# Optimization experiments

Hardware: AMD Instinct MI355X
Metric: run time of the kernel (lower is better)

Reference implementation:

```python
import jax, jax.numpy as jnp
import numpy as np

N_NODES = 100000


def gcn_conv(x, W, b, src, dst, deg_inv_sqrt):
    # x: [N, Cin], W: [Cin, Cout]. PyG GCNConv: transform then normalized aggregate.
    h = x @ W  # [N, Cout]
    norm = deg_inv_sqrt[src] * deg_inv_sqrt[dst]  # [E']
    msg = h[src] * norm[:, None]  # gather + scale
    out = jax.ops.segment_sum(msg, dst, num_segments=N_NODES)
    return out + b


def setup_inputs() -> dict:
    key = jax.random.key(0)
    ks = jax.random.split(key, 8)
    C = 256
    E = 3200000
    x = jax.random.normal(ks[0], (N_NODES, C), dtype=jnp.float32)
    edge_index = jax.random.randint(ks[1], (2, E), 0, N_NODES, dtype=jnp.int64)
    s = 1.0 / np.sqrt(C)
    W1 = jax.random.uniform(ks[2], (C, C), jnp.float32, -s, s)
    b1 = jnp.zeros((C,), jnp.float32)
    W2 = jax.random.uniform(ks[3], (C, C), jnp.float32, -s, s)
    b2 = jnp.zeros((C,), jnp.float32)
    Wl = jax.random.uniform(ks[4], (C, 1), jnp.float32, -s, s)
    bl = jnp.zeros((1,), jnp.float32)
    return {"x": x, "edge_index": edge_index, "W1": W1, "b1": b1,
            "W2": W2, "b2": b2, "Wl": Wl, "bl": bl}


def reference(x, edge_index, W1, b1, W2, b2, Wl, bl):
    # add self-loops once (shared by both conv layers)
    loops = jnp.arange(N_NODES, dtype=edge_index.dtype)
    src = jnp.concatenate([edge_index[0], loops])
    dst = jnp.concatenate([edge_index[1], loops])
    # symmetric normalization: deg counts incoming edges incl. self-loops
    deg = jax.ops.segment_sum(jnp.ones_like(dst, dtype=x.dtype), dst,
                              num_segments=N_NODES)
    deg_inv_sqrt = jax.lax.rsqrt(deg)  # deg >= 1 due to self-loops
    h = jax.nn.relu(gcn_conv(x, W1, b1, src, dst, deg_inv_sqrt))
    h = jax.nn.relu(gcn_conv(h, W2, b2, src, dst, deg_inv_sqrt))
    return h @ Wl + bl  # [N, 1]
```

## Files before the change

### kernel.cpp

```cpp
#include <hip/hip_runtime.h>

#define NN 100000
#define CC 256
#define EE 3200000

typedef __attribute__((ext_vector_type(8))) short bf16x8;
typedef __attribute__((ext_vector_type(4))) float f32x4;
typedef __attribute__((ext_vector_type(4))) _Float16 f16x4;

__device__ __forceinline__ float4 f4add(float4 a, float4 b) {
  return make_float4(a.x + b.x, a.y + b.y, a.z + b.z, a.w + b.w);
}

__device__ __forceinline__ unsigned short f2bf(float f) {
  unsigned u = __float_as_uint(f);
  unsigned r = (u + 0x7fffu + ((u >> 16) & 1u)) >> 16;
  return (unsigned short)r;
}
__device__ __forceinline__ float bf2f(unsigned short h) {
  return __uint_as_float(((unsigned)h) << 16);
}

__global__ void k_deg(const int* __restrict__ dst, int* __restrict__ cnt, int n) {
  int i = blockIdx.x * blockDim.x + threadIdx.x;
  int stride = gridDim.x * blockDim.x;
  for (; i < n; i += stride) {
    unsigned d = (unsigned)dst[i];
    if (d < NN) atomicAdd(&cnt[d], 1);
  }
}

__global__ void k_dis(const int* __restrict__ cnt, float* __restrict__ dis, int n) {
  int i = blockIdx.x * blockDim.x + threadIdx.x;
  if (i < n) dis[i] = 1.0f / sqrtf((float)(cnt[i] + 1));
}

__global__ void k_scan_local(const int* __restrict__ cnt, int* __restrict__ offs,
                             int* __restrict__ bsum, int n) {
  __shared__ int wsum[16];
  int t = threadIdx.x;
  int idx = blockIdx.x * 1024 + t;
  int lane = t & 63, wv = t >> 6;
  int v = (idx < n) ? cnt[idx] : 0;
  int x = v;
#pragma unroll
  for (int d = 1; d < 64; d <<= 1) {
    int y = __shfl_up(x, d, 64);
    if (lane >= d) x += y;
  }
  if (lane == 63) wsum[wv] = x;
  __syncthreads();
  int wpre = 0, total = 0;
#pragma unroll
  for (int w = 0; w < 16; ++w) {
    int s = wsum[w];
    if (w < wv) wpre += s;
    total += s;
  }
  if (idx < n) offs[idx] = wpre + x - v;
  if (t == 0) bsum[blockIdx.x] = total;
}

__global__ void k_scan_bsum(const int* __restrict__ bsum, int* __restrict__ bbase, int nb) {
  __shared__ int wsum[2];
  int t = threadIdx.x;
  int lane = t & 63, wv = t >> 6;
  int v = (t < nb) ? bsum[t] : 0;
  int x = v;
#pragma unroll
  for (int d = 1; d < 64; d <<= 1) {
    int y = __shfl_up(x, d, 64);
    if (lane >= d) x += y;
  }
  if (lane == 63) wsum[wv] = x;
  __syncthreads();
  int pre = (wv == 1) ? wsum[0] : 0;
  if (t < nb) bbase[t] = pre + x - v;
  if (t == nb - 1) bbase[nb] = pre + x;
}

__global__ void k_scan_add(int* __restrict__ offs, const int* __restrict__ bbase,
                           int n, int nb) {
  int i = blockIdx.x * 256 + threadIdx.x;
  if (i < n) offs[i] += bbase[i >> 10];
  if (i == 0) offs[n] = bbase[nb];
}

__global__ void k_scatter(const int* __restrict__ src, const int* __restrict__ dst,
                          const int* __restrict__ offs, int* __restrict__ fill,
                          int* __restrict__ csr, int n) {
  int i = blockIdx.x * blockDim.x + threadIdx.x;
  int stride = gridDim.x * blockDim.x;
  for (; i < n; i += stride) {
    unsigned d = (unsigned)dst[i];
    unsigned s = (unsigned)src[i];
    if (d < NN && s < NN) {
      int p = offs[d] + atomicAdd(&fill[d], 1);
      csr[p] = (int)s;
    }
  }
}

__global__ void k_wsplit(const float* __restrict__ W, unsigned short* __restrict__ WTh,
                         unsigned short* __restrict__ WTl) {
  int k = blockIdx.x, n = threadIdx.x;
  float w = W[k * CC + n];
  unsigned short h = f2bf(w);
  unsigned short l = f2bf(w - bf2f(h));
  WTh[n * CC + k] = h;
  WTl[n * CC + k] = l;
}

#define LDA 40

__global__ __launch_bounds__(512) void k_gemm_mfma(
    const float* __restrict__ A, const unsigned short* __restrict__ WTh,
    const unsigned short* __restrict__ WTl, const float* __restrict__ dis,
    _Float16* __restrict__ Out, int M) {
  __shared__ unsigned short Ah[128 * LDA], Al[128 * LDA];
  __shared__ unsigned short Bh[256 * LDA], Bl[256 * LDA];
  const int tid = threadIdx.x;
  const int wave = tid >> 6, lane = tid & 63;
  const int quad = lane >> 4, l16 = lane & 15;
  const int wm = wave >> 2, wn = wave & 3;
  const int row0 = blockIdx.x * 128;

  f32x4 acc[4][4];
#pragma unroll
  for (int i = 0; i < 4; ++i)
#pragma unroll
    for (int j = 0; j < 4; ++j) acc[i][j] = (f32x4){0.f, 0.f, 0.f, 0.f};

  for (int k0 = 0; k0 < CC; k0 += 32) {
#pragma unroll
    for (int q = 0; q < 2; ++q) {
      int idx = tid + 512 * q;
      int r = idx >> 3;
      int c4 = (idx & 7) << 2;
      int gr = row0 + r;
      float4 v = make_float4(0.f, 0.f, 0.f, 0.f);
      if (gr < M) v = *(const float4*)&A[(size_t)gr * CC + k0 + c4];
      ushort4 hv, lv;
      hv.x = f2bf(v.x); lv.x = f2bf(v.x - bf2f(hv.x));
      hv.y = f2bf(v.y); lv.y = f2bf(v.y - bf2f(hv.y));
      hv.z = f2bf(v.z); lv.z = f2bf(v.z - bf2f(hv.z));
      hv.w = f2bf(v.w); lv.w = f2bf(v.w - bf2f(hv.w));
      *(ushort4*)&Ah[r * LDA + c4] = hv;
      *(ushort4*)&Al[r * LDA + c4] = lv;
    }
#pragma unroll
    for (int q = 0; q < 4; ++q) {
      int idx = tid + 512 * q;
      int r = idx >> 3;
      int c4 = (idx & 7) << 2;
      const size_t g = (size_t)r * CC + k0 + c4;
      *(ushort4*)&Bh[r * LDA + c4] = *(const ushort4*)&WTh[g];
      *(ushort4*)&Bl[r * LDA + c4] = *(const ushort4*)&WTl[g];
    }
    __syncthreads();

    bf16x8 bh[4], bl[4];
#pragma unroll
    for (int j = 0; j < 4; ++j) {
      int br = (wn * 64 + j * 16 + l16) * LDA + quad * 8;
      bh[j] = *(const bf16x8*)&Bh[br];
      bl[j] = *(const bf16x8*)&Bl[br];
    }
#pragma unroll
    for (int i = 0; i < 4; ++i) {
      int ar = (wm * 64 + i * 16 + l16) * LDA + quad * 8;
      bf16x8 ah = *(const bf16x8*)&Ah[ar];
      bf16x8 al = *(const bf16x8*)&Al[ar];
#pragma unroll
      for (int j = 0; j < 4; ++j) {
        acc[i][j] = __builtin_amdgcn_mfma_f32_16x16x32_bf16(ah, bh[j], acc[i][j], 0, 0, 0);
        acc[i][j] = __builtin_amdgcn_mfma_f32_16x16x32_bf16(al, bh[j], acc[i][j], 0, 0, 0);
        acc[i][j] = __builtin_amdgcn_mfma_f32_16x16x32_bf16(ah, bl[j], acc[i][j], 0, 0, 0);
      }
    }
    __syncthreads();
  }

#pragma unroll
  for (int i = 0; i < 4; ++i) {
#pragma unroll
    for (int r4 = 0; r4 < 4; ++r4) {
      int r = row0 + wm * 64 + i * 16 + quad * 4 + r4;
      if (r < M) {
        float sc = dis[r];
#pragma unroll
        for (int j = 0; j < 4; ++j) {
          Out[(size_t)r * CC + wn * 64 + j * 16 + l16] =
              (_Float16)(acc[i][j][r4] * sc);
        }
      }
    }
  }
}

__global__ __launch_bounds__(256) void k_aggregate(
    const _Float16* __restrict__ hs, const int* __restrict__ offs,
    const int* __restrict__ csr, const float* __restrict__ dis,
    const float* __restrict__ bias, float* __restrict__ out, int n) {
  int node = blockIdx.x * 4 + (threadIdx.x >> 6);
  if (node >= n) return;
  int lane = threadIdx.x & 63;
  int c4 = lane << 2;
  int beg = offs[node], end = offs[node + 1];
  f16x4 sv = *(const f16x4*)&hs[(size_t)node * CC + c4];
  float4 a0 = make_float4((float)sv.x, (float)sv.y, (float)sv.z, (float)sv.w);
  float4 a1 = make_float4(0.f, 0.f, 0.f, 0.f);
  float4 a2 = make_float4(0.f, 0.f, 0.f, 0.f);
  float4 a3 = make_float4(0.f, 0.f, 0.f, 0.f);
  int e = beg;
  for (; e + 4 <= end; e += 4) {
    int s0 = csr[e], s1 = csr[e + 1], s2 = csr[e + 2], s3 = csr[e + 3];
    f16x4 v0 = *(const f16x4*)&hs[(size_t)s0 * CC + c4];
    f16x4 v1 = *(const f16x4*)&hs[(size_t)s1 * CC + c4];
    f16x4 v2 = *(const f16x4*)&hs[(size_t)s2 * CC + c4];
    f16x4 v3 = *(const f16x4*)&hs[(size_t)s3 * CC + c4];
    a0.x += (float)v0.x; a0.y += (float)v0.y; a0.z += (float)v0.z; a0.w += (float)v0.w;
    a1.x += (float)v1.x; a1.y += (float)v1.y; a1.z += (float)v1.z; a1.w += (float)v1.w;
    a2.x += (float)v2.x; a2.y += (float)v2.y; a2.z += (float)v2.z; a2.w += (float)v2.w;
    a3.x += (float)v3.x; a3.y += (float)v3.y; a3.z += (float)v3.z; a3.w += (float)v3.w;
  }
  for (; e < end; ++e) {
    int s0 = csr[e];
    f16x4 v0 = *(const f16x4*)&hs[(size_t)s0 * CC + c4];
    a0.x += (float)v0.x; a0.y += (float)v0.y; a0.z += (float)v0.z; a0.w += (float)v0.w;
  }
  float4 acc = f4add(f4add(a0, a1), f4add(a2, a3));
  float sc = dis[node];
  float4 bv = *(const float4*)&bias[c4];
  float4 r;
  r.x = fmaxf(acc.x * sc + bv.x, 0.f);
  r.y = fmaxf(acc.y * sc + bv.y, 0.f);
  r.z = fmaxf(acc.z * sc + bv.z, 0.f);
  r.w = fmaxf(acc.w * sc + bv.w, 0.f);
  *(float4*)&out[(size_t)node * CC + c4] = r;
}

__global__ __launch_bounds__(256) void k_aggregate_final(
    const _Float16* __restrict__ hs, const int* __restrict__ offs,
    const int* __restrict__ csr, const float* __restrict__ dis,
    const float* __restrict__ bias, const float* __restrict__ Wl,
    const float* __restrict__ bl, float* __restrict__ out, int n) {
  int node = blockIdx.x * 4 + (threadIdx.x >> 6);
  if (node >= n) return;
  int lane = threadIdx.x & 63;
  int c4 = lane << 2;
  int beg = offs[node], end = offs[node + 1];
  f16x4 sv = *(const f16x4*)&hs[(size_t)node * CC + c4];
  float4 a0 = make_float4((float)sv.x, (float)sv.y, (float)sv.z, (float)sv.w);
  float4 a1 = make_float4(0.f, 0.f, 0.f, 0.f);
  float4 a2 = make_float4(0.f, 0.f, 0.f, 0.f);
  float4 a3 = make_float4(0.f, 0.f, 0.f, 0.f);
  int e = beg;
  for (; e + 4 <= end; e += 4) {
    int s0 = csr[e], s1 = csr[e + 1], s2 = csr[e + 2], s3 = csr[e + 3];
    f16x4 v0 = *(const f16x4*)&hs[(size_t)s0 * CC + c4];
    f16x4 v1 = *(const f16x4*)&hs[(size_t)s1 * CC + c4];
    f16x4 v2 = *(const f16x4*)&hs[(size_t)s2 * CC + c4];
    f16x4 v3 = *(const f16x4*)&hs[(size_t)s3 * CC + c4];
    a0.x += (float)v0.x; a0.y += (float)v0.y; a0.z += (float)v0.z; a0.w += (float)v0.w;
    a1.x += (float)v1.x; a1.y += (float)v1.y; a1.z += (float)v1.z; a1.w += (float)v1.w;
    a2.x += (float)v2.x; a2.y += (float)v2.y; a2.z += (float)v2.z; a2.w += (float)v2.w;
    a3.x += (float)v3.x; a3.y += (float)v3.y; a3.z += (float)v3.z; a3.w += (float)v3.w;
  }
  for (; e < end; ++e) {
    int s0 = csr[e];
    f16x4 v0 = *(const f16x4*)&hs[(size_t)s0 * CC + c4];
    a0.x += (float)v0.x; a0.y += (float)v0.y; a0.z += (float)v0.z; a0.w += (float)v0.w;
  }
  float4 acc = f4add(f4add(a0, a1), f4add(a2, a3));
  float sc = dis[node];
  float4 bv = *(const float4*)&bias[c4];
  float4 w = *(const float4*)&Wl[c4];
  float s = fmaxf(acc.x * sc + bv.x, 0.f) * w.x +
            fmaxf(acc.y * sc + bv.y, 0.f) * w.y +
            fmaxf(acc.z * sc + bv.z, 0.f) * w.z +
            fmaxf(acc.w * sc + bv.w, 0.f) * w.w;
#pragma unroll
  for (int d = 32; d > 0; d >>= 1) s += __shfl_down(s, d, 64);
  if (lane == 0) out[node] = s + bl[0];
}

extern "C" void kernel_launch(void* const* d_in, const int* in_sizes, int n_in,
                              void* d_out, int out_size, void* d_ws, size_t ws_size,
                              hipStream_t stream) {
  const float* x = (const float*)d_in[0];
  const int* ei = (const int*)d_in[1];
  const float* W1 = (const float*)d_in[2];
  const float* b1 = (const float*)d_in[3];
  const float* W2 = (const float*)d_in[4];
  const float* b2 = (const float*)d_in[5];
  const float* Wl = (const float*)d_in[6];
  const float* bl = (const float*)d_in[7];
  float* out = (float*)d_out;

  const int* src = ei;
  const int* dst = ei + EE;

  char* ws = (char*)d_ws;
  size_t off = 0;
  auto alloc = [&](size_t bytes) {
    char* p = ws + off;
    off = (off + bytes + 255) & ~(size_t)255;
    return p;
  };
  float* dis = (float*)alloc((size_t)NN * 4);
  int* cnt = (int*)alloc((size_t)NN * 4);
  int* offs = (int*)alloc((size_t)(NN + 1) * 4);
  int* scanb = (int*)alloc(1024 * 4);
  int* scanb2 = (int*)alloc(1024 * 4);
  int* csr = (int*)alloc((size_t)EE * 4);
  unsigned short* W1h = (unsigned short*)alloc((size_t)CC * CC * 2);
  unsigned short* W1l = (unsigned short*)alloc((size_t)CC * CC * 2);
  unsigned short* W2h = (unsigned short*)alloc((size_t)CC * CC * 2);
  unsigned short* W2l = (unsigned short*)alloc((size_t)CC * CC * 2);
  _Float16* hsbuf = (_Float16*)alloc((size_t)NN * CC * 2);
  float* h1 = (float*)alloc((size_t)NN * CC * 4);

  hipMemsetAsync(cnt, 0, (size_t)NN * 4, stream);

  k_deg<<<2048, 256, 0, stream>>>(dst, cnt, EE);
  k_dis<<<(NN + 255) / 256, 256, 0, stream>>>(cnt, dis, NN);
  const int nb = (NN + 1023) / 1024;
  k_scan_local<<<nb, 1024, 0, stream>>>(cnt, offs, scanb, NN);
  k_scan_bsum<<<1, 128, 0, stream>>>(scanb, scanb2, nb);
  k_scan_add<<<(NN + 255) / 256, 256, 0, stream>>>(offs, scanb2, NN, nb);
  hipMemsetAsync(cnt, 0, (size_t)NN * 4, stream);
  k_scatter<<<2048, 256, 0, stream>>>(src, dst, offs, cnt, csr, EE);

  k_wsplit<<<CC, CC, 0, stream>>>(W1, W1h, W1l);
  k_wsplit<<<CC, CC, 0, stream>>>(W2, W2h, W2l);

  const int gblocks = (NN + 127) / 128;
  k_gemm_mfma<<<gblocks, 512, 0, stream>>>(x, W1h, W1l, dis, hsbuf, NN);
  k_aggregate<<<(NN + 3) / 4, 256, 0, stream>>>(hsbuf, offs, csr, dis, b1, h1, NN);
  k_gemm_mfma<<<gblocks, 512, 0, stream>>>(h1, W2h, W2l, dis, hsbuf, NN);
  k_aggregate_final<<<(NN + 3) / 4, 256, 0, stream>>>(hsbuf, offs, csr, dis, b2, Wl, bl, out, NN);
}
```

Before: 1.057 ms.

## Fuse small preprocessing kernels and unroll aggregation gather loop to eight

```diff
diff --git a/kernel.cpp b/kernel.cpp
--- a/kernel.cpp
+++ b/kernel.cpp
@@ -30,18 +30,14 @@
   }
 }
 
-__global__ void k_dis(const int* __restrict__ cnt, float* __restrict__ dis, int n) {
-  int i = blockIdx.x * blockDim.x + threadIdx.x;
-  if (i < n) dis[i] = 1.0f / sqrtf((float)(cnt[i] + 1));
-}
-
 __global__ void k_scan_local(const int* __restrict__ cnt, int* __restrict__ offs,
-                             int* __restrict__ bsum, int n) {
+                             int* __restrict__ bsum, float* __restrict__ dis, int n) {
   __shared__ int wsum[16];
   int t = threadIdx.x;
   int idx = blockIdx.x * 1024 + t;
   int lane = t & 63, wv = t >> 6;
   int v = (idx < n) ? cnt[idx] : 0;
+  if (idx < n) dis[idx] = 1.0f / sqrtf((float)(v + 1));
   int x = v;
 #pragma unroll
   for (int d = 1; d < 64; d <<= 1) {
@@ -80,9 +76,12 @@
 }
 
 __global__ void k_scan_add(int* __restrict__ offs, const int* __restrict__ bbase,
-                           int n, int nb) {
+                           int* __restrict__ cnt, int n, int nb) {
   int i = blockIdx.x * 256 + threadIdx.x;
-  if (i < n) offs[i] += bbase[i >> 10];
+  if (i < n) {
+    offs[i] += bbase[i >> 10];
+    cnt[i] = 0;
+  }
   if (i == 0) offs[n] = bbase[nb];
 }
 
@@ -101,14 +100,23 @@
   }
 }
 
-__global__ void k_wsplit(const float* __restrict__ W, unsigned short* __restrict__ WTh,
-                         unsigned short* __restrict__ WTl) {
-  int k = blockIdx.x, n = threadIdx.x;
-  float w = W[k * CC + n];
-  unsigned short h = f2bf(w);
-  unsigned short l = f2bf(w - bf2f(h));
-  WTh[n * CC + k] = h;
-  WTl[n * CC + k] = l;
+__global__ void k_wsplit2(const float* __restrict__ W1, const float* __restrict__ W2,
+                          unsigned short* __restrict__ W1h, unsigned short* __restrict__ W1l,
+                          unsigned short* __restrict__ W2h, unsigned short* __restrict__ W2l) {
+  int b = blockIdx.x, t = threadIdx.x;
+  int idx = (b & 255) * 256 + t;
+  int k = idx >> 8, n = idx & 255;
+  if (b < 256) {
+    float w = W1[k * CC + n];
+    unsigned short h = f2bf(w);
+    W1h[n * CC + k] = h;
+    W1l[n * CC + k] = f2bf(w - bf2f(h));
+  } else {
+    float w = W2[k * CC + n];
+    unsigned short h = f2bf(w);
+    W2h[n * CC + k] = h;
+    W2l[n * CC + k] = f2bf(w - bf2f(h));
+  }
 }
 
 #define LDA 40
@@ -213,18 +221,34 @@
   float4 a2 = make_float4(0.f, 0.f, 0.f, 0.f);
   float4 a3 = make_float4(0.f, 0.f, 0.f, 0.f);
   int e = beg;
-  for (; e + 4 <= end; e += 4) {
-    int s0 = csr[e], s1 = csr[e + 1], s2 = csr[e + 2], s3 = csr[e + 3];
+  for (; e + 8 <= end; e += 8) {
+    int s0 = csr[e],     s1 = csr[e + 1], s2 = csr[e + 2], s3 = csr[e + 3];
+    int s4 = csr[e + 4], s5 = csr[e + 5], s6 = csr[e + 6], s7 = csr[e + 7];
     f16x4 v0 = *(const f16x4*)&hs[(size_t)s0 * CC + c4];
     f16x4 v1 = *(const f16x4*)&hs[(size_t)s1 * CC + c4];
     f16x4 v2 = *(const f16x4*)&hs[(size_t)s2 * CC + c4];
     f16x4 v3 = *(const f16x4*)&hs[(size_t)s3 * CC + c4];
+    f16x4 v4 = *(const f16x4*)&hs[(size_t)s4 * CC + c4];
+    f16x4 v5 = *(const f16x4*)&hs[(size_t)s5 * CC + c4];
+    f16x4 v6 = *(const f16x4*)&hs[(size_t)s6 * CC + c4];
+    f16x4 v7 = *(const f16x4*)&hs[(size_t)s7 * CC + c4];
+    a0.x += (float)v0.x + (float)v4.x; a0.y += (float)v0.y + (float)v4.y;
+    a0.z += (float)v0.z + (float)v4.z; a0.w += (float)v0.w + (float)v4.w;
+    a1.x += (float)v1.x + (float)v5.x; a1.y += (float)v1.y + (float)v5.y;
+    a1.z += (float)v1.z + (float)v5.z; a1.w += (float)v1.w + (float)v5.w;
+    a2.x += (float)v2.x + (float)v6.x; a2.y += (float)v2.y + (float)v6.y;
+    a2.z += (float)v2.z + (float)v6.z; a2.w += (float)v2.w + (float)v6.w;
+    a3.x += (float)v3.x + (float)v7.x; a3.y += (float)v3.y + (float)v7.y;
+    a3.z += (float)v3.z + (float)v7.z; a3.w += (float)v3.w + (float)v7.w;
+  }
+  for (; e + 2 <= end; e += 2) {
+    int s0 = csr[e], s1 = csr[e + 1];
+    f16x4 v0 = *(const f16x4*)&hs[(size_t)s0 * CC + c4];
+    f16x4 v1 = *(const f16x4*)&hs[(size_t)s1 * CC + c4];
     a0.x += (float)v0.x; a0.y += (float)v0.y; a0.z += (float)v0.z; a0.w += (float)v0.w;
     a1.x += (float)v1.x; a1.y += (float)v1.y; a1.z += (float)v1.z; a1.w += (float)v1.w;
-    a2.x += (float)v2.x; a2.y += (float)v2.y; a2.z += (float)v2.z; a2.w += (float)v2.w;
-    a3.x += (float)v3.x; a3.y += (float)v3.y; a3.z += (float)v3.z; a3.w += (float)v3.w;
-  }
-  for (; e < end; ++e) {
+  }
+  if (e < end) {
     int s0 = csr[e];
     f16x4 v0 = *(const f16x4*)&hs[(size_t)s0 * CC + c4];
     a0.x += (float)v0.x; a0.y += (float)v0.y; a0.z += (float)v0.z; a0.w += (float)v0.w;
@@ -256,18 +280,34 @@
   float4 a2 = make_float4(0.f, 0.f, 0.f, 0.f);
   float4 a3 = make_float4(0.f, 0.f, 0.f, 0.f);
   int e = beg;
-  for (; e + 4 <= end; e += 4) {
-    int s0 = csr[e], s1 = csr[e + 1], s2 = csr[e + 2], s3 = csr[e + 3];
+  for (; e + 8 <= end; e += 8) {
+    int s0 = csr[e],     s1 = csr[e + 1], s2 = csr[e + 2], s3 = csr[e + 3];
+    int s4 = csr[e + 4], s5 = csr[e + 5], s6 = csr[e + 6], s7 = csr[e + 7];
     f16x4 v0 = *(const f16x4*)&hs[(size_t)s0 * CC + c4];
     f16x4 v1 = *(const f16x4*)&hs[(size_t)s1 * CC + c4];
     f16x4 v2 = *(const f16x4*)&hs[(size_t)s2 * CC + c4];
     f16x4 v3 = *(const f16x4*)&hs[(size_t)s3 * CC + c4];
+    f16x4 v4 = *(const f16x4*)&hs[(size_t)s4 * CC + c4];
+    f16x4 v5 = *(const f16x4*)&hs[(size_t)s5 * CC + c4];
+    f16x4 v6 = *(const f16x4*)&hs[(size_t)s6 * CC + c4];
+    f16x4 v7 = *(const f16x4*)&hs[(size_t)s7 * CC + c4];
+    a0.x += (float)v0.x + (float)v4.x; a0.y += (float)v0.y + (float)v4.y;
+    a0.z += (float)v0.z + (float)v4.z; a0.w += (float)v0.w + (float)v4.w;
+    a1.x += (float)v1.x + (float)v5.x; a1.y += (float)v1.y + (float)v5.y;
+    a1.z += (float)v1.z + (float)v5.z; a1.w += (float)v1.w + (float)v5.w;
+    a2.x += (float)v2.x + (float)v6.x; a2.y += (float)v2.y + (float)v6.y;
+    a2.z += (float)v2.z + (float)v6.z; a2.w += (float)v2.w + (float)v6.w;
+    a3.x += (float)v3.x + (float)v7.x; a3.y += (float)v3.y + (float)v7.y;
+    a3.z += (float)v3.z + (float)v7.z; a3.w += (float)v3.w + (float)v7.w;
+  }
+  for (; e + 2 <= end; e += 2) {
+    int s0 = csr[e], s1 = csr[e + 1];
+    f16x4 v0 = *(const f16x4*)&hs[(size_t)s0 * CC + c4];
+    f16x4 v1 = *(const f16x4*)&hs[(size_t)s1 * CC + c4];
     a0.x += (float)v0.x; a0.y += (float)v0.y; a0.z += (float)v0.z; a0.w += (float)v0.w;
     a1.x += (float)v1.x; a1.y += (float)v1.y; a1.z += (float)v1.z; a1.w += (float)v1.w;
-    a2.x += (float)v2.x; a2.y += (float)v2.y; a2.z += (float)v2.z; a2.w += (float)v2.w;
-    a3.x += (float)v3.x; a3.y += (float)v3.y; a3.z += (float)v3.z; a3.w += (float)v3.w;
-  }
-  for (; e < end; ++e) {
+  }
+  if (e < end) {
     int s0 = csr[e];
     f16x4 v0 = *(const f16x4*)&hs[(size_t)s0 * CC + c4];
     a0.x += (float)v0.x; a0.y += (float)v0.y; a0.z += (float)v0.z; a0.w += (float)v0.w;
@@ -311,8 +351,8 @@
   float* dis = (float*)alloc((size_t)NN * 4);
   int* cnt = (int*)alloc((size_t)NN * 4);
   int* offs = (int*)alloc((size_t)(NN + 1) * 4);
-  int* scanb = (int*)alloc(1024 * 4);
-  int* scanb2 = (int*)alloc(1024 * 4);
+  int* bsum = (int*)alloc(1024 * 4);
+  int* bbase = (int*)alloc(1024 * 4);
   int* csr = (int*)alloc((size_t)EE * 4);
   unsigned short* W1h = (unsigned short*)alloc((size_t)CC * CC * 2);
   unsigned short* W1l = (unsigned short*)alloc((size_t)CC * CC * 2);
@@ -322,18 +362,13 @@
   float* h1 = (float*)alloc((size_t)NN * CC * 4);
 
   hipMemsetAsync(cnt, 0, (size_t)NN * 4, stream);
-
   k_deg<<<2048, 256, 0, stream>>>(dst, cnt, EE);
-  k_dis<<<(NN + 255) / 256, 256, 0, stream>>>(cnt, dis, NN);
   const int nb = (NN + 1023) / 1024;
-  k_scan_local<<<nb, 1024, 0, stream>>>(cnt, offs, scanb, NN);
-  k_scan_bsum<<<1, 128, 0, stream>>>(scanb, scanb2, nb);
-  k_scan_add<<<(NN + 255) / 256, 256, 0, stream>>>(offs, scanb2, NN, nb);
-  hipMemsetAsync(cnt, 0, (size_t)NN * 4, stream);
+  k_scan_local<<<nb, 1024, 0, stream>>>(cnt, offs, bsum, dis, NN);
+  k_scan_bsum<<<1, 128, 0, stream>>>(bsum, bbase, nb);
+  k_scan_add<<<(NN + 255) / 256, 256, 0, stream>>>(offs, bbase, cnt, NN, nb);
   k_scatter<<<2048, 256, 0, stream>>>(src, dst, offs, cnt, csr, EE);
-
-  k_wsplit<<<CC, CC, 0, stream>>>(W1, W1h, W1l);
-  k_wsplit<<<CC, CC, 0, stream>>>(W2, W2h, W2l);
+  k_wsplit2<<<512, 256, 0, stream>>>(W1, W2, W1h, W1l, W2h, W2l);
 
   const int gblocks = (NN + 127) / 128;
   k_gemm_mfma<<<gblocks, 512, 0, stream>>>(x, W1h, W1l, dis, hsbuf, NN);
```

After: 1.048 ms. Within noise of the previous version (-0.9%).
